# Kernel tuning notes

Measured on AMD Instinct MI355X. Metric: run time of the kernel, lower is better.

The kernel has to match this reference:

```python
import jax, jax.numpy as jnp
import numpy as np

N = 8192
D_IN = 256
D_OUT = 256
DROP_P = 0.5


def setup_inputs() -> dict:
    key = jax.random.key(0)
    k1, k2, k3, k4, k5 = jax.random.split(key, 5)
    inputs = jax.random.normal(k1, (N, D_IN), dtype=jnp.float32)
    # torch nn.Linear weights are [d_out, d_in], applied as x @ W.T
    Wq = jax.random.normal(k2, (D_OUT, D_IN), dtype=jnp.float32) * (1.0 / np.sqrt(D_IN))
    Wk = jax.random.normal(k3, (D_OUT, D_IN), dtype=jnp.float32) * (1.0 / np.sqrt(D_IN))
    Wv = jax.random.normal(k4, (D_OUT, D_IN), dtype=jnp.float32) * (1.0 / np.sqrt(D_IN))
    # deterministic dropout keep-mask (True = keep), p=0.5
    drop_mask = jax.random.bernoulli(k5, 1.0 - DROP_P, (N, N))
    return {"inputs": inputs, "Wq": Wq, "Wk": Wk, "Wv": Wv, "drop_mask": drop_mask}


def reference(inputs, Wq, Wk, Wv, drop_mask):
    # QKV projections (no bias)
    q = inputs @ Wq.T  # [N, d_out]
    k = inputs @ Wk.T  # [N, d_out]
    v = inputs @ Wv.T  # [N, d_out]

    d_k = k.shape[1]
    scores = q @ k.T  # [N, N]

    # causal mask: strictly-upper-triangular entries -> -inf
    n = scores.shape[0]
    causal = jnp.triu(jnp.ones((n, n), dtype=bool), k=1)
    masked = jnp.where(causal, -jnp.inf, scores)

    attn_weights = jax.nn.softmax(masked / jnp.sqrt(jnp.float32(d_k)), axis=-1)

    # dropout p=0.5 in train mode: zero dropped entries, scale kept by 1/(1-p)
    scale = jnp.float32(1.0 / (1.0 - DROP_P))
    attn_weights = jnp.where(drop_mask, attn_weights * scale, 0.0)

    context_vector = attn_weights @ v  # [N, d_out]
    return context_vector
```

## Files before the change

kernel.cpp:

```cpp
#include <hip/hip_runtime.h>

#define NT 8192
#define DM 256

typedef float f32x16 __attribute__((ext_vector_type(16)));
typedef float f32x4 __attribute__((ext_vector_type(4)));
typedef __bf16 bf16x8 __attribute__((ext_vector_type(8)));

#define MFMA32(a, b, c) __builtin_amdgcn_mfma_f32_32x32x16_bf16((a), (b), (c), 0, 0, 0)
#define MFMA16(a, b, c) __builtin_amdgcn_mfma_f32_16x16x32_bf16((a), (b), (c), 0, 0, 0)
#define NEG_INF (-__builtin_inff())

static __device__ __forceinline__ unsigned short f2bf_bits(float f) {
  return __builtin_bit_cast(unsigned short, (__bf16)f);
}
static __device__ __forceinline__ float exp2_fast(float x) {
  return __builtin_amdgcn_exp2f(x);
}
static __device__ __forceinline__ void gload_lds16(const void* g, void* l) {
  __builtin_amdgcn_global_load_lds(
      (const __attribute__((address_space(1))) unsigned int*)g,
      (__attribute__((address_space(3))) unsigned int*)l, 16, 0, 0);
}

__global__ __launch_bounds__(256) void maskpack_kernel(
    const void* __restrict__ mask, unsigned long long* __restrict__ bm) {
  const int t = threadIdx.x, lane = t & 63, w = t >> 6;
  const int r = blockIdx.x + (w << 11);
  const unsigned int* md = (const unsigned int*)mask;
  bool a01 = true, af = true;
#pragma unroll
  for (int k = 0; k < 4; ++k) {
    unsigned int v = md[lane + 64 * k];
    a01 = a01 && (v <= 1u);
    af = af && (v == 0u || v == 0x3F800000u);
  }
  const bool dword_mode = __all(a01) || __all(af);
  unsigned long long* out = bm + (size_t)r * 128;
  if (dword_mode) {
    const unsigned int* mk = (const unsigned int*)mask + (size_t)r * NT;
    const int iters = (r >> 8) + 1;
    for (int it = 0; it < iters; ++it) {
      const int j0 = it * 256;
      unsigned int v0 = mk[j0 + lane];
      unsigned int v1 = mk[j0 + 64 + lane];
      unsigned int v2 = mk[j0 + 128 + lane];
      unsigned int v3 = mk[j0 + 192 + lane];
      unsigned long long b0 = __ballot(v0 != 0u);
      unsigned long long b1 = __ballot(v1 != 0u);
      unsigned long long b2 = __ballot(v2 != 0u);
      unsigned long long b3 = __ballot(v3 != 0u);
      if (lane == 0) {
        out[(j0 >> 6) + 0] = b0;
        out[(j0 >> 6) + 1] = b1;
        out[(j0 >> 6) + 2] = b2;
        out[(j0 >> 6) + 3] = b3;
      }
    }
  } else {
    const unsigned char* mk = (const unsigned char*)mask + (size_t)r * NT;
    unsigned short* outs = (unsigned short*)out;
    const int iters = (r >> 10) + 1;
    for (int it = 0; it < iters; ++it) {
      const uint4 d = *(const uint4*)(mk + it * 1024 + lane * 16);
      unsigned int dws[4] = {d.x, d.y, d.z, d.w};
      unsigned int m16 = 0;
#pragma unroll
      for (int k = 0; k < 4; ++k) {
        unsigned int x = dws[k];
        x |= x >> 4;
        x |= x >> 2;
        x |= x >> 1;
        x &= 0x01010101u;
        m16 |= ((x * 0x01020408u) >> 24) << (4 * k);
      }
      outs[it * 64 + lane] = (unsigned short)m16;
    }
  }
}

__global__ __launch_bounds__(256) void proj_kernel(
    const float* __restrict__ X, const float* __restrict__ Wq,
    const float* __restrict__ Wk, const float* __restrict__ Wv,
    unsigned short* __restrict__ Qs, unsigned short* __restrict__ Kb,
    unsigned short* __restrict__ Vt) {
  __shared__ __align__(16) unsigned short Xs[64 * 256];
  __shared__ __align__(16) unsigned short Ws[64 * 256];
  __shared__ float Tr[4][32 * 33];
  const int ib = blockIdx.x, mat = blockIdx.y;
  const float* W = (mat == 0) ? Wq : (mat == 1) ? Wk : Wv;
  const float wscale = (mat == 0) ? 0.09016844005556021f : (mat == 2 ? 2.0f : 1.0f);
  const int t = threadIdx.x;
  const int lane = t & 63, w = t >> 6;
  const int m = lane & 31, half = lane >> 5;
  const int i0 = ib * 64;
#pragma unroll
  for (int cc = 0; cc < 8; ++cc) {
    int chunk = t + 256 * cc;
    int rr = chunk >> 5, c = chunk & 31;
    const float4* src = (const float4*)(X + (size_t)(i0 + rr) * 256 + c * 8);
    float4 f0 = src[0], f1 = src[1];
    bf16x8 v;
    v[0] = (__bf16)f0.x; v[1] = (__bf16)f0.y; v[2] = (__bf16)f0.z; v[3] = (__bf16)f0.w;
    v[4] = (__bf16)f1.x; v[5] = (__bf16)f1.y; v[6] = (__bf16)f1.z; v[7] = (__bf16)f1.w;
    *(bf16x8*)&Xs[(rr * 32 + (c ^ (rr & 31))) * 8] = v;
  }
  const int wr = w >> 1, wc = w & 1;
  for (int cb = 0; cb < 4; ++cb) {
    __syncthreads();
#pragma unroll
    for (int cc = 0; cc < 8; ++cc) {
      int chunk = t + 256 * cc;
      int rr = chunk >> 5, c = chunk & 31;
      const float4* src = (const float4*)(W + (size_t)(cb * 64 + rr) * 256 + c * 8);
      float4 f0 = src[0], f1 = src[1];
      bf16x8 v;
      v[0] = (__bf16)(f0.x * wscale); v[1] = (__bf16)(f0.y * wscale);
      v[2] = (__bf16)(f0.z * wscale); v[3] = (__bf16)(f0.w * wscale);
      v[4] = (__bf16)(f1.x * wscale); v[5] = (__bf16)(f1.y * wscale);
      v[6] = (__bf16)(f1.z * wscale); v[7] = (__bf16)(f1.w * wscale);
      *(bf16x8*)&Ws[(rr * 32 + (c ^ (rr & 31))) * 8] = v;
    }
    __syncthreads();
    f32x16 acc = {};
    const int ar = 32 * wr + m;
    const int br = 32 * wc + m;
#pragma unroll
    for (int st = 0; st < 16; ++st) {
      int kc = st * 2 + half;
      bf16x8 a = *(const bf16x8*)&Xs[(ar * 32 + (kc ^ (ar & 31))) * 8];
      bf16x8 b = *(const bf16x8*)&Ws[(br * 32 + (kc ^ (br & 31))) * 8];
      acc = MFMA32(a, b, acc);
    }
    if (mat < 2) {
      unsigned short* O = mat ? Kb : Qs;
#pragma unroll
      for (int r = 0; r < 16; ++r) {
        int row = i0 + 32 * wr + (r & 3) + 8 * (r >> 2) + 4 * half;
        int col = cb * 64 + 32 * wc + m;
        O[(size_t)row * DM + col] = f2bf_bits(acc[r]);
      }
    } else {
      float* T = Tr[w];
#pragma unroll
      for (int r = 0; r < 16; ++r) {
        int rl = (r & 3) + 8 * (r >> 2) + 4 * half;
        T[m * 33 + rl] = acc[r];
      }
      asm volatile("s_waitcnt lgkmcnt(0)" ::: "memory");
#pragma unroll
      for (int q = 0; q < 16; ++q) {
        int dl = 2 * q + half;
        float val = T[dl * 33 + m];
        Vt[(size_t)(cb * 64 + 32 * wc + dl) * NT + i0 + 32 * wr + m] = f2bf_bits(val);
      }
      asm volatile("s_waitcnt lgkmcnt(0)" ::: "memory");
    }
  }
}

__global__ __launch_bounds__(256, 2) void flash_kernel(
    const unsigned short* __restrict__ Qs, const unsigned short* __restrict__ Kg,
    const unsigned short* __restrict__ Vtg, const unsigned int* __restrict__ bm,
    float* __restrict__ ml_out, unsigned short* __restrict__ acc_out) {
  __shared__ __align__(16) unsigned short Ksh[2][32 * 256];
  __shared__ __align__(16) unsigned short Vsh[2][256 * 32];
  __shared__ __align__(16) unsigned short Psh[4][16 * 40];
  const int ib = blockIdx.x;
  const int seg = blockIdx.y;
  const int jb_end = 2 * (ib + 1);
  const int jb0 = seg * 16;
  if (jb0 >= jb_end) return;
  const int jb1 = (jb0 + 16 < jb_end) ? jb0 + 16 : jb_end;
  const int t = threadIdx.x, lane = t & 63, w = t >> 6;
  const int m = lane & 15, q = lane >> 4;
  const int i0 = ib * 64, rw0 = i0 + 16 * w;
  const int myrow = rw0 + m;

  bf16x8 qf[8];
  {
    const unsigned short* qp = Qs + (size_t)myrow * DM + q * 8;
#pragma unroll
    for (int st = 0; st < 8; ++st) qf[st] = *(const bf16x8*)(qp + st * 32);
  }
  f32x4 oacc[16] = {};
  float mrun = -1e30f, lrun = 0.f;

#define STAGE(JB, B)                                                          \
  {                                                                           \
    const int j32_ = (JB) * 32;                                               \
    _Pragma("unroll") for (int i_ = 0; i_ < 4; ++i_) {                        \
      int chunk = t + 256 * i_;                                               \
      int row = chunk >> 5, slot = chunk & 31;                                \
      gload_lds16(Kg + (size_t)(j32_ + row) * DM + (slot ^ row) * 8,          \
                  &Ksh[B][(size_t)chunk * 8]);                                \
    }                                                                         \
    _Pragma("unroll") for (int i_ = 0; i_ < 4; ++i_) {                        \
      int chunk = t + 256 * i_;                                               \
      int d_ = chunk >> 2, slot = chunk & 3;                                  \
      gload_lds16(Vtg + (size_t)d_ * NT + j32_ + (slot ^ (d_ & 3)) * 8,       \
                  &Vsh[B][(size_t)chunk * 8]);                                \
    }                                                                         \
  }

  STAGE(jb0, 0)
  unsigned int bits = bm[(size_t)myrow * 256 + jb0];
  for (int jb = jb0; jb < jb1; ++jb) {
    const int buf = (jb - jb0) & 1;
    const int j32 = jb * 32;
    asm volatile("s_waitcnt vmcnt(0)" ::: "memory");
    __builtin_amdgcn_s_barrier();
    unsigned int bits_next = 0;
    if (jb + 1 < jb1) {
      STAGE(jb + 1, buf ^ 1)
      bits_next = bm[(size_t)myrow * 256 + jb + 1];
    }
    if (j32 <= rw0 + 15) {
      const unsigned short* Kb_ = Ksh[buf];
      const unsigned short* Vb_ = Vsh[buf];
      f32x4 s[2] = {};
#pragma unroll
      for (int st = 0; st < 8; ++st) {
        int kc = st * 4 + q;
#pragma unroll
        for (int ct = 0; ct < 2; ++ct) {
          int jr = ct * 16 + m;
          bf16x8 a = *(const bf16x8*)&Kb_[(jr * 32 + (kc ^ jr)) * 8];
          s[ct] = MFMA16(a, qf[st], s[ct]);
        }
      }
      if (j32 + 31 > rw0) {
#pragma unroll
        for (int ct = 0; ct < 2; ++ct)
#pragma unroll
          for (int r = 0; r < 4; ++r)
            if (j32 + ct * 16 + q * 4 + r > myrow) s[ct][r] = NEG_INF;
      }
      float mx = fmaxf(fmaxf(fmaxf(s[0][0], s[0][1]), fmaxf(s[0][2], s[0][3])),
                       fmaxf(fmaxf(s[1][0], s[1][1]), fmaxf(s[1][2], s[1][3])));
      mx = fmaxf(mx, __shfl_xor(mx, 16));
      mx = fmaxf(mx, __shfl_xor(mx, 32));
      const float mn = fmaxf(mrun, mx);
#pragma unroll
      for (int ct = 0; ct < 2; ++ct)
#pragma unroll
        for (int r = 0; r < 4; ++r) s[ct][r] = exp2_fast(s[ct][r] - mn);
      float rs = (s[0][0] + s[0][1]) + (s[0][2] + s[0][3]) +
                 (s[1][0] + s[1][1]) + (s[1][2] + s[1][3]);
      rs += __shfl_xor(rs, 16);
      rs += __shfl_xor(rs, 32);
      if (__all(mn == mrun)) {
        lrun += rs;
      } else {
        float alpha = exp2_fast(mrun - mn);
        lrun = lrun * alpha + rs;
#pragma unroll
        for (int ct = 0; ct < 16; ++ct)
#pragma unroll
          for (int r = 0; r < 4; ++r) oacc[ct][r] *= alpha;
        mrun = mn;
      }
      unsigned short* P = Psh[w];
#pragma unroll
      for (int ct = 0; ct < 2; ++ct) {
        unsigned int bb = bits >> (ct * 16 + q * 4);
        unsigned long long pk = 0;
#pragma unroll
        for (int r = 0; r < 4; ++r) {
          float pv = ((bb >> r) & 1u) ? s[ct][r] : 0.0f;
          pk |= (unsigned long long)f2bf_bits(pv) << (16 * r);
        }
        int c = ct * 2 + (q >> 1);
        *(unsigned long long*)&P[m * 40 + c * 8 + ((q & 1) << 2)] = pk;
      }
      asm volatile("s_waitcnt lgkmcnt(0)" ::: "memory");
      bf16x8 pf = *(const bf16x8*)&P[m * 40 + q * 8];
#pragma unroll
      for (int ct = 0; ct < 16; ++ct) {
        int d = ct * 16 + m;
        bf16x8 a = *(const bf16x8*)&Vb_[(d * 4 + (q ^ (d & 3))) * 8];
        oacc[ct] = MFMA16(a, pf, oacc[ct]);
      }
    }
    bits = bits_next;
  }
#undef STAGE
  const int a_ = ib >> 3, r_ = ib & 7;
  const int g = 4 * a_ * (a_ + 1) + r_ * (a_ + 1) + seg;
  if (q == 0) {
    float* mlb = ml_out + ((size_t)g * 64 + 16 * w + m) * 2;
    mlb[0] = mrun;
    mlb[1] = lrun;
  }
  unsigned short* ab = acc_out + ((size_t)g * 64 + 16 * w + m) * DM;
#pragma unroll
  for (int ct = 0; ct < 16; ++ct) {
    unsigned long long pk = 0;
#pragma unroll
    for (int r = 0; r < 4; ++r)
      pk |= (unsigned long long)f2bf_bits(oacc[ct][r]) << (16 * r);
    *(unsigned long long*)&ab[ct * 16 + q * 4] = pk;
  }
}

__global__ __launch_bounds__(256) void combine_kernel(
    const float* __restrict__ ml, const unsigned short* __restrict__ pacc,
    float* __restrict__ out) {
  const int t = threadIdx.x;
  const int row = blockIdx.x * 32 + (t >> 3);
  const int cg = (t & 7) * 32;
  const int ib = row >> 6, rib = row & 63;
  const int a = ib >> 3, r = ib & 7;
  const int g0 = 4 * a * (a + 1) + r * (a + 1);
  const int ns = a + 1;
  float M = -1e30f;
  for (int s = 0; s < ns; ++s) M = fmaxf(M, ml[((size_t)(g0 + s) * 64 + rib) * 2]);
  float Wd = 0.f;
  float acc[32];
#pragma unroll
  for (int j = 0; j < 32; ++j) acc[j] = 0.f;
  for (int s = 0; s < ns; ++s) {
    const float* mls = ml + ((size_t)(g0 + s) * 64 + rib) * 2;
    float wv = exp2_fast(mls[0] - M);
    Wd += wv * mls[1];
    const unsigned short* pa = pacc + ((size_t)(g0 + s) * 64 + rib) * DM + cg;
#pragma unroll
    for (int v4 = 0; v4 < 4; ++v4) {
      bf16x8 b = *(const bf16x8*)(pa + v4 * 8);
#pragma unroll
      for (int j = 0; j < 8; ++j) acc[v4 * 8 + j] += wv * (float)b[j];
    }
  }
  float inv = 1.0f / Wd;
#pragma unroll
  for (int j = 0; j < 32; ++j) out[(size_t)row * DM + cg + j] = acc[j] * inv;
}

extern "C" void kernel_launch(void* const* d_in, const int* in_sizes, int n_in,
                              void* d_out, int out_size, void* d_ws, size_t ws_size,
                              hipStream_t stream) {
  const float* X  = (const float*)d_in[0];
  const float* Wq = (const float*)d_in[1];
  const float* Wk = (const float*)d_in[2];
  const float* Wv = (const float*)d_in[3];
  const void* mask = d_in[4];
  float* out = (float*)d_out;

  char* ws = (char*)d_ws;
  unsigned short* Qs = (unsigned short*)(ws + 4096);
  unsigned short* Kb = Qs + (size_t)NT * DM;
  unsigned short* Vt = Kb + (size_t)NT * DM;
  float* ml = (float*)(Vt + (size_t)NT * DM);
  unsigned short* pacc = (unsigned short*)(ml + (size_t)1088 * 64 * 2);
  unsigned long long* bmw = (unsigned long long*)((char*)pacc + (size_t)1088 * 64 * DM * 2);

  maskpack_kernel<<<2048, 256, 0, stream>>>(mask, bmw);
  proj_kernel<<<dim3(128, 3), 256, 0, stream>>>(X, Wq, Wk, Wv, Qs, Kb, Vt);
  flash_kernel<<<dim3(128, 16), 256, 0, stream>>>(Qs, Kb, Vt, (const unsigned int*)bmw,
                                                  ml, pacc);
  combine_kernel<<<256, 256, 0, stream>>>(ml, pacc, out);
}
```

Baseline: 476.5 us.

## Single-buffer K/V tiles, shuffle-based P transpose, raise occupancy to three blocks

After: 467.1 us. 2.0% less time.

```diff
diff --git a/kernel.cpp b/kernel.cpp
--- a/kernel.cpp
+++ b/kernel.cpp
@@ -6,6 +6,7 @@
 typedef float f32x16 __attribute__((ext_vector_type(16)));
 typedef float f32x4 __attribute__((ext_vector_type(4)));
 typedef __bf16 bf16x8 __attribute__((ext_vector_type(8)));
+typedef unsigned int u32x4 __attribute__((ext_vector_type(4)));
 
 #define MFMA32(a, b, c) __builtin_amdgcn_mfma_f32_32x32x16_bf16((a), (b), (c), 0, 0, 0)
 #define MFMA16(a, b, c) __builtin_amdgcn_mfma_f32_16x16x32_bf16((a), (b), (c), 0, 0, 0)
@@ -159,13 +160,12 @@
   }
 }
 
-__global__ __launch_bounds__(256, 2) void flash_kernel(
+__global__ __launch_bounds__(256, 3) void flash_kernel(
     const unsigned short* __restrict__ Qs, const unsigned short* __restrict__ Kg,
     const unsigned short* __restrict__ Vtg, const unsigned int* __restrict__ bm,
     float* __restrict__ ml_out, unsigned short* __restrict__ acc_out) {
-  __shared__ __align__(16) unsigned short Ksh[2][32 * 256];
-  __shared__ __align__(16) unsigned short Vsh[2][256 * 32];
-  __shared__ __align__(16) unsigned short Psh[4][16 * 40];
+  __shared__ __align__(16) unsigned short Ksh[32 * 256];
+  __shared__ __align__(16) unsigned short Vsh[256 * 32];
   const int ib = blockIdx.x;
   const int seg = blockIdx.y;
   const int jb_end = 2 * (ib + 1);
@@ -186,38 +186,29 @@
   f32x4 oacc[16] = {};
   float mrun = -1e30f, lrun = 0.f;
 
-#define STAGE(JB, B)                                                          \
+#define STAGE(JB)                                                             \
   {                                                                           \
     const int j32_ = (JB) * 32;                                               \
     _Pragma("unroll") for (int i_ = 0; i_ < 4; ++i_) {                        \
       int chunk = t + 256 * i_;                                               \
       int row = chunk >> 5, slot = chunk & 31;                                \
       gload_lds16(Kg + (size_t)(j32_ + row) * DM + (slot ^ row) * 8,          \
-                  &Ksh[B][(size_t)chunk * 8]);                                \
+                  Ksh + (size_t)chunk * 8);                                   \
     }                                                                         \
     _Pragma("unroll") for (int i_ = 0; i_ < 4; ++i_) {                        \
       int chunk = t + 256 * i_;                                               \
       int d_ = chunk >> 2, slot = chunk & 3;                                  \
       gload_lds16(Vtg + (size_t)d_ * NT + j32_ + (slot ^ (d_ & 3)) * 8,       \
-                  &Vsh[B][(size_t)chunk * 8]);                                \
+                  Vsh + (size_t)chunk * 8);                                   \
     }                                                                         \
   }
 
-  STAGE(jb0, 0)
+  STAGE(jb0)
   unsigned int bits = bm[(size_t)myrow * 256 + jb0];
   for (int jb = jb0; jb < jb1; ++jb) {
-    const int buf = (jb - jb0) & 1;
     const int j32 = jb * 32;
-    asm volatile("s_waitcnt vmcnt(0)" ::: "memory");
-    __builtin_amdgcn_s_barrier();
-    unsigned int bits_next = 0;
-    if (jb + 1 < jb1) {
-      STAGE(jb + 1, buf ^ 1)
-      bits_next = bm[(size_t)myrow * 256 + jb + 1];
-    }
+    __syncthreads();
     if (j32 <= rw0 + 15) {
-      const unsigned short* Kb_ = Ksh[buf];
-      const unsigned short* Vb_ = Vsh[buf];
       f32x4 s[2] = {};
 #pragma unroll
       for (int st = 0; st < 8; ++st) {
@@ -225,7 +216,7 @@
 #pragma unroll
         for (int ct = 0; ct < 2; ++ct) {
           int jr = ct * 16 + m;
-          bf16x8 a = *(const bf16x8*)&Kb_[(jr * 32 + (kc ^ jr)) * 8];
+          bf16x8 a = *(const bf16x8*)&Ksh[(jr * 32 + (kc ^ jr)) * 8];
           s[ct] = MFMA16(a, qf[st], s[ct]);
         }
       }
@@ -260,29 +251,45 @@
           for (int r = 0; r < 4; ++r) oacc[ct][r] *= alpha;
         mrun = mn;
       }
-      unsigned short* P = Psh[w];
-#pragma unroll
-      for (int ct = 0; ct < 2; ++ct) {
-        unsigned int bb = bits >> (ct * 16 + q * 4);
-        unsigned long long pk = 0;
-#pragma unroll
-        for (int r = 0; r < 4; ++r) {
-          float pv = ((bb >> r) & 1u) ? s[ct][r] : 0.0f;
-          pk |= (unsigned long long)f2bf_bits(pv) << (16 * r);
-        }
-        int c = ct * 2 + (q >> 1);
-        *(unsigned long long*)&P[m * 40 + c * 8 + ((q & 1) << 2)] = pk;
-      }
-      asm volatile("s_waitcnt lgkmcnt(0)" ::: "memory");
-      bf16x8 pf = *(const bf16x8*)&P[m * 40 + q * 8];
+      unsigned int A0, A1, B0, B1;
+      {
+        unsigned int bbA = bits >> (q * 4);
+        unsigned int bbB = bits >> (16 + q * 4);
+        float a0 = (bbA & 1u) ? s[0][0] : 0.f, a1 = (bbA & 2u) ? s[0][1] : 0.f;
+        float a2 = (bbA & 4u) ? s[0][2] : 0.f, a3 = (bbA & 8u) ? s[0][3] : 0.f;
+        float b0 = (bbB & 1u) ? s[1][0] : 0.f, b1 = (bbB & 2u) ? s[1][1] : 0.f;
+        float b2 = (bbB & 4u) ? s[1][2] : 0.f, b3 = (bbB & 8u) ? s[1][3] : 0.f;
+        A0 = (unsigned)f2bf_bits(a0) | ((unsigned)f2bf_bits(a1) << 16);
+        A1 = (unsigned)f2bf_bits(a2) | ((unsigned)f2bf_bits(a3) << 16);
+        B0 = (unsigned)f2bf_bits(b0) | ((unsigned)f2bf_bits(b1) << 16);
+        B1 = (unsigned)f2bf_bits(b2) | ((unsigned)f2bf_bits(b3) << 16);
+      }
+      unsigned int own0 = (q & 2) ? B0 : A0, own1 = (q & 2) ? B1 : A1;
+      unsigned int sA0 = (q & 2) ? A0 : B0, sA1 = (q & 2) ? A1 : B1;
+      unsigned int r10 = __shfl_xor(sA0, 32);
+      unsigned int r11 = __shfl_xor(sA1, 32);
+      const bool selOwn = ((q ^ (q >> 1)) & 1) != 0;
+      unsigned int s20 = selOwn ? own0 : r10;
+      unsigned int s21 = selOwn ? own1 : r11;
+      unsigned int r20 = __shfl_xor(s20, 16);
+      unsigned int r21 = __shfl_xor(s21, 16);
+      unsigned int lo0 = (q == 0) ? own0 : (q == 2) ? r10 : r20;
+      unsigned int lo1 = (q == 0) ? own1 : (q == 2) ? r11 : r21;
+      unsigned int hi0 = (q == 3) ? own0 : (q == 1) ? r10 : r20;
+      unsigned int hi1 = (q == 3) ? own1 : (q == 1) ? r11 : r21;
+      bf16x8 pf = __builtin_bit_cast(bf16x8, (u32x4){lo0, lo1, hi0, hi1});
 #pragma unroll
       for (int ct = 0; ct < 16; ++ct) {
         int d = ct * 16 + m;
-        bf16x8 a = *(const bf16x8*)&Vb_[(d * 4 + (q ^ (d & 3))) * 8];
+        bf16x8 a = *(const bf16x8*)&Vsh[(d * 4 + (q ^ (d & 3))) * 8];
         oacc[ct] = MFMA16(a, pf, oacc[ct]);
       }
     }
-    bits = bits_next;
+    __syncthreads();
+    if (jb + 1 < jb1) {
+      STAGE(jb + 1)
+      bits = bm[(size_t)myrow * 256 + jb + 1];
+    }
   }
 #undef STAGE
   const int a_ = ib >> 3, r_ = ib & 7;
```
